# Kernel optimization log

Measured on AMD Instinct MI355X. Metric: run time of the kernel, lower is better.

The kernel has to match this reference:

```python
import jax, jax.numpy as jnp
import numpy as np

TOPK = 8
EPS = 1e-12  # F.normalize eps


def setup_inputs() -> dict:
    key = jax.random.key(0)
    k1, k2 = jax.random.split(key)
    feats = jax.random.normal(k1, (4, 256, 64, 64), dtype=jnp.float32)
    logits = jax.random.normal(k2, (4, 1, 64, 64), dtype=jnp.float32)
    return {"feats": feats, "logits": logits}


def reference(feats, logits):
    b, c, h, w = feats.shape
    n = h * w
    feat_flat = feats.reshape(b, c, n)
    # F.normalize(dim=1): x / max(||x||_2, eps)
    norm = jnp.sqrt(jnp.sum(feat_flat * feat_flat, axis=1, keepdims=True))
    feat_norm = feat_flat / jnp.maximum(norm, EPS)
    # sim[b,i,j] = <f_i, f_j>  -> [B, N, N]
    sim = jnp.einsum('bci,bcj->bij', feat_norm, feat_norm)
    k = min(TOPK, n)
    _, idx = jax.lax.top_k(sim, k)  # [B, N, k] indices
    prob = jax.nn.sigmoid(logits).reshape(b, n)  # [B, N]
    # gathered[b,i,j] = prob[b, idx[b,i,j]]
    gathered = jax.vmap(lambda p, i: p[i])(prob, idx)  # [B, N, k]
    anchor = prob[:, :, None]  # [B, N, 1] broadcast over k
    loss = jnp.mean(jnp.abs(anchor - gathered))
    return loss
```

## Files before the change

kernel.cpp:

```cpp
#include <hip/hip_runtime.h>
#include <hip/hip_bf16.h>

typedef _Float16 half8 __attribute__((ext_vector_type(8)));
typedef unsigned short ushort8 __attribute__((ext_vector_type(8)));
typedef float floatx4 __attribute__((ext_vector_type(4)));

#define B_ 4
#define C_ 256
#define N_ 4096
#define NT 32
#define TRI 528

#define OFF_FN    ((size_t)0)
#define OFF_PROB  ((size_t)(8u << 20))
#define OFF_PART  (OFF_PROB + 65536)
#define OFF_TOP   ((size_t)(16u << 20))

__device__ __forceinline__ void gl_lds16(const void* g, void* l) {
    __builtin_amdgcn_global_load_lds(
        (const __attribute__((address_space(1))) void*)g,
        (__attribute__((address_space(3))) void*)l,
        16, 0, 0);
}

__device__ __forceinline__ void cas(uint32_t& a, uint32_t& b) {
    uint32_t hi = max(a, b); b = min(a, b); a = hi;
}

__device__ __forceinline__ void sort8(uint32_t v[8]) {
    cas(v[0],v[1]); cas(v[2],v[3]); cas(v[4],v[5]); cas(v[6],v[7]);
    cas(v[0],v[2]); cas(v[1],v[3]); cas(v[4],v[6]); cas(v[5],v[7]);
    cas(v[1],v[2]); cas(v[5],v[6]);
    cas(v[0],v[4]); cas(v[1],v[5]); cas(v[2],v[6]); cas(v[3],v[7]);
    cas(v[2],v[4]); cas(v[3],v[5]);
    cas(v[1],v[2]); cas(v[3],v[4]); cas(v[5],v[6]);
}

__device__ __forceinline__ void merge8(uint32_t r[8], const uint32_t n[8]) {
    uint32_t m[8];
#pragma unroll
    for (int i = 0; i < 8; ++i) m[i] = max(r[i], n[7 - i]);
    cas(m[0],m[4]); cas(m[1],m[5]); cas(m[2],m[6]); cas(m[3],m[7]);
    cas(m[0],m[2]); cas(m[1],m[3]); cas(m[4],m[6]); cas(m[5],m[7]);
    cas(m[0],m[1]); cas(m[2],m[3]); cas(m[4],m[5]); cas(m[6],m[7]);
#pragma unroll
    for (int i = 0; i < 8; ++i) r[i] = m[i];
}

#define TS 68
__global__ __launch_bounds__(1024) void prep_kernel(const float* __restrict__ feats,
                                                    const float* __restrict__ logits,
                                                    _Float16* __restrict__ fn,
                                                    float* __restrict__ prob) {
    __shared__ __align__(16) float T[C_ * TS];
    __shared__ float S[256];
    __shared__ float I[64];

    const int t  = threadIdx.x;
    const int b  = blockIdx.x >> 6;
    const int i0 = (blockIdx.x & 63) * 64;
    const float* fb = feats + (size_t)b * C_ * N_;

#pragma unroll
    for (int k = 0; k < 4; ++k) {
        int idx = t + k * 1024;
        int row = idx >> 4, col4 = idx & 15;
        float4 v = *(const float4*)(fb + (size_t)row * N_ + i0 + col4 * 4);
        *(float4*)&T[row * TS + col4 * 4] = v;
    }
    __syncthreads();
    if (t < 256) {
        int i = t & 63, cq = t >> 6;
        float ss = 0.f;
#pragma unroll 8
        for (int j = 0; j < 64; ++j) { float v = T[(cq * 64 + j) * TS + i]; ss += v * v; }
        S[cq * 64 + i] = ss;
    }
    __syncthreads();
    if (t < 64) {
        float ss = S[t] + S[64 + t] + S[128 + t] + S[192 + t];
        I[t] = 1.f / fmaxf(sqrtf(ss), 1e-12f);
        float lg = logits[b * N_ + i0 + t];
        prob[b * N_ + i0 + t] = 1.f / (1.f + expf(-lg));
    }
    __syncthreads();
    {
        int i = t >> 4, sub = t & 15;
        float s = I[i];
        _Float16* fr = fn + ((size_t)(b * N_ + i0 + i)) * C_ + sub * 16;
#pragma unroll
        for (int v8 = 0; v8 < 2; ++v8) {
            half8 h;
#pragma unroll
            for (int e = 0; e < 8; ++e)
                h[e] = (_Float16)(T[(sub * 16 + v8 * 8 + e) * TS + i] * s);
            *(half8*)(fr + v8 * 8) = h;
        }
    }
}

#define CSH 136
__global__ __launch_bounds__(256, 3) void gram_sel_kernel(const _Float16* __restrict__ fn,
                                                          uint32_t* __restrict__ top) {
    __shared__ __align__(16) char smem[128 * CSH * 2];
    unsigned short* Ch = (unsigned short*)smem;
    uint32_t* Ms = (uint32_t*)smem;

    const int t    = threadIdx.x;
    const int lane = t & 63;
    const int w    = t >> 6;
    const int m16  = lane & 15;
    const int q    = lane >> 4;

    const int bid0 = blockIdx.x;
    const int bid  = (bid0 & 7) * 264 + (bid0 >> 3);

    const int b = bid / TRI;
    const int u = bid - b * TRI;
    int it = (int)(32.5f - sqrtf(32.5f * 32.5f - 2.0f * (float)u));
    while (u >= (it + 1) * (65 - (it + 1)) / 2) ++it;
    while (u < it * (65 - it) / 2) --it;
    const int jt = it + (u - it * (65 - it) / 2);
    const bool diag = (it == jt);

    const int i0 = it * 128, j0 = jt * 128;
    const _Float16* fnb = fn + (size_t)b * N_ * C_;

    const int rbase = t >> 2;
    const int sch8  = ((t & 3) ^ (rbase & 3)) * 8;

    floatx4 acc[2][8];
#pragma unroll
    for (int ri = 0; ri < 2; ++ri)
#pragma unroll
        for (int jj = 0; jj < 8; ++jj) acc[ri][jj] = floatx4{0.f, 0.f, 0.f, 0.f};

    auto stage = [&](int kc8, int bsel) {
        char* base = smem + bsel * 16384;
#pragma unroll
        for (int rr = 0; rr < 2; ++rr) {
            int row = rr * 64 + rbase;
            const _Float16* gA = fnb + (size_t)(i0 + row) * C_ + kc8 * 32 + sch8;
            const _Float16* gB = fnb + (size_t)(j0 + row) * C_ + kc8 * 32 + sch8;
            gl_lds16(gA, base + rr * 4096 + t * 16);
            gl_lds16(gB, base + 8192 + rr * 4096 + t * 16);
        }
    };
    auto compute = [&](int bsel) {
        const _Float16* Asb = (const _Float16*)(smem + bsel * 16384);
        const _Float16* Bsb = Asb + 4096;
        const int co = (q ^ (m16 & 3)) * 8;
        half8 a0 = *(const half8*)&Asb[(w * 32 + m16) * 32 + co];
        half8 a1 = *(const half8*)&Asb[(w * 32 + 16 + m16) * 32 + co];
#pragma unroll
        for (int jj = 0; jj < 8; ++jj) {
            half8 bf = *(const half8*)&Bsb[(jj * 16 + m16) * 32 + co];
            acc[0][jj] = __builtin_amdgcn_mfma_f32_16x16x32_f16(a0, bf, acc[0][jj], 0, 0, 0);
            acc[1][jj] = __builtin_amdgcn_mfma_f32_16x16x32_f16(a1, bf, acc[1][jj], 0, 0, 0);
        }
    };

    stage(0, 0);
    __syncthreads();
#pragma unroll
    for (int s = 0; s < 8; ++s) {
        if (s < 7) stage(s + 1, (s + 1) & 1);
        compute(s & 1);
        __syncthreads();
    }

#pragma unroll
    for (int jj = 0; jj < 8; ++jj)
#pragma unroll
        for (int ri = 0; ri < 2; ++ri) {
            const int col = jj * 16 + m16;
            const int row = w * 32 + ri * 16 + q * 4;
#pragma unroll
            for (int p = 0; p < 2; ++p) {
                auto pk2 = __builtin_amdgcn_cvt_pkrtz(acc[ri][jj][2 * p], acc[ri][jj][2 * p + 1]);
                uint32_t bits = __builtin_bit_cast(uint32_t, pk2);
                uint32_t s = (bits >> 15) & 0x00010001u;
                uint32_t fl = bits ^ (s * 0x7FFFu + 0x80008000u);
                *(uint32_t*)&Ch[col * CSH + row + 2 * p] = fl;
            }
        }
    __syncthreads();

    uint32_t cpk[8], rpk[8];
    {
        const int ccol = t >> 1, cr0 = (t & 1) * 64;
        const unsigned short* cc = &Ch[ccol * CSH + cr0];
        const int ibase = i0 + cr0;
#pragma unroll
        for (int g = 0; g < 8; ++g) {
            ushort8 v = *(const ushort8*)(cc + g * 8);
            uint32_t cand[8];
#pragma unroll
            for (int e = 0; e < 8; ++e)
                cand[e] = ((uint32_t)v[e] << 16) | (uint32_t)(ibase + g * 8 + e);
            sort8(cand);
            if (g == 0) {
#pragma unroll
                for (int s = 0; s < 8; ++s) cpk[s] = cand[s];
            } else merge8(cpk, cand);
        }
    }
    if (!diag) {
        const int rrow = t >> 1, ch0 = (t & 1) * 64;
        const unsigned short* cr = &Ch[ch0 * CSH + rrow];
        const int jbase = j0 + ch0;
#pragma unroll
        for (int g = 0; g < 8; ++g) {
            uint32_t cand[8];
#pragma unroll
            for (int e = 0; e < 8; ++e)
                cand[e] = ((uint32_t)cr[(g * 8 + e) * CSH] << 16) | (uint32_t)(jbase + g * 8 + e);
            sort8(cand);
            if (g == 0) {
#pragma unroll
                for (int s = 0; s < 8; ++s) rpk[s] = cand[s];
            } else merge8(rpk, cand);
        }
    }
    __syncthreads();

    if (t & 1) {
#pragma unroll
        for (int s = 0; s < 8; ++s) Ms[(t >> 1) * 8 + s] = cpk[s];
        if (!diag) {
#pragma unroll
            for (int s = 0; s < 8; ++s) Ms[1024 + (t >> 1) * 8 + s] = rpk[s];
        }
    }
    __syncthreads();
    if (!(t & 1)) {
        uint32_t o[8];
#pragma unroll
        for (int s = 0; s < 8; ++s) o[s] = Ms[(t >> 1) * 8 + s];
        merge8(cpk, o);
        uint32_t* dst = top + (((size_t)b * N_ + j0 + (t >> 1)) * 32 + it) * 8;
        *(uint4*)dst       = make_uint4(cpk[0], cpk[1], cpk[2], cpk[3]);
        *(uint4*)(dst + 4) = make_uint4(cpk[4], cpk[5], cpk[6], cpk[7]);
        if (!diag) {
#pragma unroll
            for (int s = 0; s < 8; ++s) o[s] = Ms[1024 + (t >> 1) * 8 + s];
            merge8(rpk, o);
            uint32_t* dst2 = top + (((size_t)b * N_ + i0 + (t >> 1)) * 32 + jt) * 8;
            *(uint4*)dst2       = make_uint4(rpk[0], rpk[1], rpk[2], rpk[3]);
            *(uint4*)(dst2 + 4) = make_uint4(rpk[4], rpk[5], rpk[6], rpk[7]);
        }
    }
}

__global__ __launch_bounds__(256) void merge_kernel(const uint32_t* __restrict__ top,
                                                    const float* __restrict__ prob,
                                                    float* __restrict__ partials) {
    __shared__ float red[4];
    const int t = threadIdx.x;
    const int lane = t & 63;
    const int w = t >> 6;
    const int rg = blockIdx.x * 4 + w;
    const int b = rg >> 12;

    uint4 v4 = ((const uint4*)(top + (size_t)rg * 256))[lane];
    uint32_t v[4] = {v4.x, v4.y, v4.z, v4.w};
    uint32_t m = max(max(v[0], v[1]), max(v[2], v[3]));

    const float* pb = prob + (b << 12);
    float p_r = prob[rg];
    float contrib = 0.f;
#pragma unroll
    for (int k = 0; k < 8; ++k) {
        uint32_t M = m;
#pragma unroll
        for (int off = 32; off; off >>= 1) M = max(M, (uint32_t)__shfl_xor((int)M, off));
        if (lane == k) contrib = fabsf(p_r - pb[M & 0xFFFu]);
#pragma unroll
        for (int s = 0; s < 4; ++s) v[s] = (v[s] == M) ? 0u : v[s];
        m = max(max(v[0], v[1]), max(v[2], v[3]));
    }
#pragma unroll
    for (int off = 32; off; off >>= 1) contrib += __shfl_xor(contrib, off);
    if (lane == 0) red[w] = contrib;
    __syncthreads();
    if (t == 0) partials[blockIdx.x] = red[0] + red[1] + red[2] + red[3];
}

__global__ __launch_bounds__(256) void final_kernel(const float* __restrict__ partials,
                                                    float* __restrict__ out) {
    __shared__ float red[256];
    int t = threadIdx.x;
    float s = 0.f;
#pragma unroll
    for (int k = 0; k < 16; ++k) s += partials[k * 256 + t];
    red[t] = s;
    __syncthreads();
    for (int off = 128; off > 0; off >>= 1) {
        if (t < off) red[t] += red[t + off];
        __syncthreads();
    }
    if (t == 0) out[0] = red[0] * (1.f / (B_ * N_ * 8.0f));
}

extern "C" void kernel_launch(void* const* d_in, const int* in_sizes, int n_in,
                              void* d_out, int out_size, void* d_ws, size_t ws_size,
                              hipStream_t stream) {
    const float* feats  = (const float*)d_in[0];
    const float* logits = (const float*)d_in[1];
    float* out = (float*)d_out;
    char* ws = (char*)d_ws;
    _Float16* fn   = (_Float16*)(ws + OFF_FN);
    float* prob    = (float*)(ws + OFF_PROB);
    float* parts   = (float*)(ws + OFF_PART);
    uint32_t* top  = (uint32_t*)(ws + OFF_TOP);

    prep_kernel<<<256, 1024, 0, stream>>>(feats, logits, fn, prob);
    gram_sel_kernel<<<B_ * TRI, 256, 0, stream>>>(fn, top);
    merge_kernel<<<4096, 256, 0, stream>>>(top, prob, parts);
    final_kernel<<<1, 256, 0, stream>>>(parts, out);
}
```

Measured before the change: 125.7 us.

## Repack gram LDS tile as paired rows with 8-way XOR swizzle; shrink prep blocks

```diff
diff --git a/kernel.cpp b/kernel.cpp
--- a/kernel.cpp
+++ b/kernel.cpp
@@ -48,10 +48,10 @@
 }
 
 #define TS 68
-__global__ __launch_bounds__(1024) void prep_kernel(const float* __restrict__ feats,
-                                                    const float* __restrict__ logits,
-                                                    _Float16* __restrict__ fn,
-                                                    float* __restrict__ prob) {
+__global__ __launch_bounds__(256) void prep_kernel(const float* __restrict__ feats,
+                                                   const float* __restrict__ logits,
+                                                   _Float16* __restrict__ fn,
+                                                   float* __restrict__ prob) {
     __shared__ __align__(16) float T[C_ * TS];
     __shared__ float S[256];
     __shared__ float I[64];
@@ -62,14 +62,14 @@
     const float* fb = feats + (size_t)b * C_ * N_;
 
 #pragma unroll
-    for (int k = 0; k < 4; ++k) {
-        int idx = t + k * 1024;
-        int row = idx >> 4, col4 = idx & 15;
+    for (int k = 0; k < 16; ++k) {
+        int ch = t + k * 256;
+        int row = ch >> 4, col4 = ch & 15;
         float4 v = *(const float4*)(fb + (size_t)row * N_ + i0 + col4 * 4);
         *(float4*)&T[row * TS + col4 * 4] = v;
     }
     __syncthreads();
-    if (t < 256) {
+    {
         int i = t & 63, cq = t >> 6;
         float ss = 0.f;
 #pragma unroll 8
@@ -85,15 +85,15 @@
     }
     __syncthreads();
     {
-        int i = t >> 4, sub = t & 15;
+        int i = t >> 2, chunk = t & 3;
         float s = I[i];
-        _Float16* fr = fn + ((size_t)(b * N_ + i0 + i)) * C_ + sub * 16;
-#pragma unroll
-        for (int v8 = 0; v8 < 2; ++v8) {
+        _Float16* fr = fn + ((size_t)(b * N_ + i0 + i)) * C_ + chunk * 64;
+#pragma unroll
+        for (int v8 = 0; v8 < 8; ++v8) {
             half8 h;
 #pragma unroll
             for (int e = 0; e < 8; ++e)
-                h[e] = (_Float16)(T[(sub * 16 + v8 * 8 + e) * TS + i] * s);
+                h[e] = (_Float16)(T[(chunk * 64 + v8 * 8 + e) * TS + i] * s);
             *(half8*)(fr + v8 * 8) = h;
         }
     }
@@ -126,8 +126,11 @@
     const int i0 = it * 128, j0 = jt * 128;
     const _Float16* fnb = fn + (size_t)b * N_ * C_;
 
-    const int rbase = t >> 2;
-    const int sch8  = ((t & 3) ^ (rbase & 3)) * 8;
+    const int sR  = t >> 3;
+    const int s8  = t & 7;
+    const int slg = s8 ^ (sR & 7);
+    const int sp  = slg >> 2;
+    const int sc  = slg & 3;
 
     floatx4 acc[2][8];
 #pragma unroll
@@ -139,9 +142,9 @@
         char* base = smem + bsel * 16384;
 #pragma unroll
         for (int rr = 0; rr < 2; ++rr) {
-            int row = rr * 64 + rbase;
-            const _Float16* gA = fnb + (size_t)(i0 + row) * C_ + kc8 * 32 + sch8;
-            const _Float16* gB = fnb + (size_t)(j0 + row) * C_ + kc8 * 32 + sch8;
+            int row = rr * 64 + 2 * sR + sp;
+            const _Float16* gA = fnb + (size_t)(i0 + row) * C_ + kc8 * 32 + sc * 8;
+            const _Float16* gB = fnb + (size_t)(j0 + row) * C_ + kc8 * 32 + sc * 8;
             gl_lds16(gA, base + rr * 4096 + t * 16);
             gl_lds16(gB, base + 8192 + rr * 4096 + t * 16);
         }
@@ -149,12 +152,13 @@
     auto compute = [&](int bsel) {
         const _Float16* Asb = (const _Float16*)(smem + bsel * 16384);
         const _Float16* Bsb = Asb + 4096;
-        const int co = (q ^ (m16 & 3)) * 8;
-        half8 a0 = *(const half8*)&Asb[(w * 32 + m16) * 32 + co];
-        half8 a1 = *(const half8*)&Asb[(w * 32 + 16 + m16) * 32 + co];
+        const int hh   = m16 >> 1;
+        const int slot = (((((m16 & 1) << 2) | q) ^ hh)) * 8;
+        half8 a0 = *(const half8*)&Asb[(w * 16 + hh) * 64 + slot];
+        half8 a1 = *(const half8*)&Asb[(w * 16 + 8 + hh) * 64 + slot];
 #pragma unroll
         for (int jj = 0; jj < 8; ++jj) {
-            half8 bf = *(const half8*)&Bsb[(jj * 16 + m16) * 32 + co];
+            half8 bf = *(const half8*)&Bsb[(jj * 8 + hh) * 64 + slot];
             acc[0][jj] = __builtin_amdgcn_mfma_f32_16x16x32_f16(a0, bf, acc[0][jj], 0, 0, 0);
             acc[1][jj] = __builtin_amdgcn_mfma_f32_16x16x32_f16(a1, bf, acc[1][jj], 0, 0, 0);
         }
@@ -314,7 +318,7 @@
     float* parts   = (float*)(ws + OFF_PART);
     uint32_t* top  = (uint32_t*)(ws + OFF_TOP);
 
-    prep_kernel<<<256, 1024, 0, stream>>>(feats, logits, fn, prob);
+    prep_kernel<<<256, 256, 0, stream>>>(feats, logits, fn, prob);
     gram_sel_kernel<<<B_ * TRI, 256, 0, stream>>>(fn, top);
     merge_kernel<<<4096, 256, 0, stream>>>(top, prob, parts);
     final_kernel<<<1, 256, 0, stream>>>(parts, out);
```

Result: no change. 125.3 us (-0.3%).
